# Kernel tuning notes

Hardware: AMD Instinct MI355X
Metric: run time of the kernel (lower is better)

Reference implementation:

```python
import jax, jax.numpy as jnp
import numpy as np

_POWERS = jnp.array([128, 64, 32, 16, 8, 4, 2, 1], dtype=jnp.int32)


def _unpack_ternary(pos_mask, neg_mask, in_dim):
    """Unpack uint8-style bitmasks [out, in//8] to ternary {-1,0,+1} [out, in]."""
    out_dim = pos_mask.shape[0]
    pos_bits = ((pos_mask[:, :, None] & _POWERS) != 0).astype(jnp.int8)  # [out, in/8, 8]
    neg_bits = ((neg_mask[:, :, None] & _POWERS) != 0).astype(jnp.int8)
    w_t = (pos_bits - neg_bits).reshape(out_dim, -1)[:, :in_dim]
    return w_t


def setup_inputs() -> dict:
    key = jax.random.key(0)
    k1, k2, k3, k4, k5 = jax.random.split(key, 5)
    TOKENS, IN, OUT = 4096, 4096, 4096
    x = jax.random.normal(k1, (TOKENS, IN), dtype=jnp.float32)
    pos_mask = jax.random.randint(k2, (OUT, IN // 8), 0, 256, dtype=jnp.int32)
    neg_mask = jax.random.randint(k3, (OUT, IN // 8), 0, 256, dtype=jnp.int32)
    scale = jax.random.uniform(k4, (), dtype=jnp.float32) * 0.05 + 0.01  # absmean scale
    bias = jax.random.normal(k5, (OUT,), dtype=jnp.float32)
    return {"x": x, "pos_mask": pos_mask, "neg_mask": neg_mask, "scale": scale,
            "bias": bias, "in_features": IN}


def reference(x, pos_mask, neg_mask, scale, bias, in_features):
    # y = scale * (x @ W_pos.T - x @ W_neg.T) + bias == scale * (x @ w_t.T) + bias,
    # since pos - neg == w_t exactly (entries in {-1,0,+1}).
    w_t = _unpack_ternary(pos_mask, neg_mask, in_features).astype(x.dtype)  # [out, in]
    y = scale * jnp.einsum('ti,oi->to', x, w_t) + bias
    return y
```

## Files before the change

### kernel.cpp

```cpp
#include <hip/hip_runtime.h>
#include <hip/hip_bf16.h>

typedef unsigned short ushort_t;
typedef unsigned int uint_t;

typedef __attribute__((ext_vector_type(8))) short bf16x8;
typedef __attribute__((ext_vector_type(4))) float f32x4;
typedef __attribute__((ext_vector_type(8))) unsigned short u16x8;

constexpr int Mdim = 4096;
constexpr int Ndim = 4096;
constexpr int Kdim = 4096;
constexpr int K2 = Kdim * 2;
constexpr int NIT = Kdim / 128;

__device__ __forceinline__ ushort_t f2bf(float f) {
  uint_t u = __float_as_uint(f);
  u += 0x7fffu + ((u >> 16) & 1u);
  return (ushort_t)(u >> 16);
}

__global__ void __launch_bounds__(256) cvt_x_kernel(const float* __restrict__ x,
                                                    ushort_t* __restrict__ xb) {
  const size_t t = (size_t)blockIdx.x * 256 + threadIdx.x;
  const float4* p = reinterpret_cast<const float4*>(x) + t * 2;
  float4 a = p[0], b = p[1];
  u16x8 o;
  o[0] = f2bf(a.x); o[1] = f2bf(a.y); o[2] = f2bf(a.z); o[3] = f2bf(a.w);
  o[4] = f2bf(b.x); o[5] = f2bf(b.y); o[6] = f2bf(b.z); o[7] = f2bf(b.w);
  *reinterpret_cast<u16x8*>(xb + t * 8) = o;
}

__global__ void __launch_bounds__(256) unpack_w_kernel(const int* __restrict__ pos,
                                                       const int* __restrict__ neg,
                                                       ushort_t* __restrict__ wb) {
  const size_t t = (size_t)blockIdx.x * 256 + threadIdx.x;
  const int4 p = reinterpret_cast<const int4*>(pos)[t];
  const int4 q = reinterpret_cast<const int4*>(neg)[t];
  const int pv[4] = {p.x, p.y, p.z, p.w};
  const int nv[4] = {q.x, q.y, q.z, q.w};
  ushort_t* dst = wb + t * 32;
#pragma unroll
  for (int e = 0; e < 4; ++e) {
    u16x8 v;
#pragma unroll
    for (int j = 0; j < 8; ++j) {
      const int pb = (pv[e] >> (7 - j)) & 1;
      const int nb = (nv[e] >> (7 - j)) & 1;
      const int d = pb - nb;
      v[j] = (d == 1) ? (ushort_t)0x3F80 : ((d == -1) ? (ushort_t)0xBF80 : (ushort_t)0);
    }
    *reinterpret_cast<u16x8*>(dst + e * 8) = v;
  }
}

#define GLD16(gp, lp)                                                     \
  __builtin_amdgcn_global_load_lds(                                       \
      (const __attribute__((address_space(1))) void*)(gp),                \
      (__attribute__((address_space(3))) void*)(lp), 16, 0, 0)

#define VMCNT(N) asm volatile("s_waitcnt vmcnt(" #N ")" ::: "memory")

#define BARRIER() do {                          \
  __builtin_amdgcn_sched_barrier(0);            \
  __builtin_amdgcn_s_barrier();                 \
  __builtin_amdgcn_sched_barrier(0);            \
} while (0)


#define STAGE_A(BUF, HALF, KT) do {                                                    \
  const char* g_ = Ab + gAoff + (size_t)(HALF) * (128 * (size_t)K2) + (size_t)(KT) * 128; \
  char* l_ = ldsw + (BUF) * 32768 + (HALF) * 16384;                                    \
  GLD16(g_, l_);                                                                       \
  GLD16(g_ + (size_t)64 * K2, l_ + 8192);                                              \
} while (0)

#define STAGE_B(BUF, HALF, KT) do {                                                    \
  const char* g_ = Bb + gBoff + (size_t)(HALF) * (128 * (size_t)K2) + (size_t)(KT) * 128; \
  char* l_ = ldsw + 65536 + (BUF) * 32768 + (HALF) * 16384;                            \
  GLD16(g_, l_);                                                                       \
  GLD16(g_ + (size_t)64 * K2, l_ + 8192);                                              \
} while (0)

#define LDA(BUF, M, KK) (*(const bf16x8*)(lds + (BUF) * 32768 + aRowBase + (M) * 2048 + acol[KK]))
#define LDB(BUF, N, KK) (*(const bf16x8*)(lds + 65536 + (BUF) * 32768 + bRowBase + (N) * 2048 + acol[KK]))

#define PHASE(BUF, Q, PREBAR2, ...) do {                                               \
  bf16x8 a0k0 = LDA(BUF, 2*(Q),   0), a0k1 = LDA(BUF, 2*(Q),   1);                     \
  bf16x8 a1k0 = LDA(BUF, 2*(Q)+1, 0), a1k1 = LDA(BUF, 2*(Q)+1, 1);                     \
  if ((Q) == 0) {                                                                      \
    _Pragma("unroll")                                                                  \
    for (int n_ = 0; n_ < 4; ++n_) { vb[n_][0] = LDB(BUF, n_, 0); vb[n_][1] = LDB(BUF, n_, 1); } \
  }                                                                                    \
  __VA_ARGS__;                                                                         \
  BARRIER();                                                                           \
  __builtin_amdgcn_s_setprio(1);                                                       \
  _Pragma("unroll")                                                                    \
  for (int n_ = 0; n_ < 4; ++n_) {                                                     \
    acc[2*(Q)][n_]   = __builtin_amdgcn_mfma_f32_16x16x32_bf16(a0k0, vb[n_][0], acc[2*(Q)][n_],   0, 0, 0); \
    acc[2*(Q)+1][n_] = __builtin_amdgcn_mfma_f32_16x16x32_bf16(a1k0, vb[n_][0], acc[2*(Q)+1][n_], 0, 0, 0); \
  }                                                                                    \
  _Pragma("unroll")                                                                    \
  for (int n_ = 0; n_ < 4; ++n_) {                                                     \
    acc[2*(Q)][n_]   = __builtin_amdgcn_mfma_f32_16x16x32_bf16(a0k1, vb[n_][1], acc[2*(Q)][n_],   0, 0, 0); \
    acc[2*(Q)+1][n_] = __builtin_amdgcn_mfma_f32_16x16x32_bf16(a1k1, vb[n_][1], acc[2*(Q)+1][n_], 0, 0, 0); \
  }                                                                                    \
  __builtin_amdgcn_s_setprio(0);                                                       \
  PREBAR2;                                                                             \
  BARRIER();                                                                           \
} while (0)

__global__ void __launch_bounds__(512, 2) gemm_kernel(const ushort_t* __restrict__ A,
                                                      const ushort_t* __restrict__ B,
                                                      float* __restrict__ C,
                                                      const float* __restrict__ scale_p,
                                                      const float* __restrict__ bias) {
  __shared__ char lds[131072];

  const int bid = blockIdx.x;
  const int swz = (bid & 7) * 32 + (bid >> 3);
  const int m0 = (swz >> 4) * 256;
  const int n0 = (swz & 15) * 256;

  const int tid = threadIdx.x;
  const int wid = tid >> 6;
  const int lane = tid & 63;
  const int wr = wid >> 2;
  const int wc = wid & 3;

  float sv = *scale_p;
  float bv[4];
#pragma unroll
  for (int n = 0; n < 4; ++n) bv[n] = bias[n0 + wc * 64 + n * 16 + (lane & 15)];
  asm volatile("" : "+v"(sv), "+v"(bv[0]), "+v"(bv[1]), "+v"(bv[2]), "+v"(bv[3]));

  const int srow = tid >> 3;
  const int scol = 16 * ((tid & 7) ^ (srow & 7));
  const char* Ab = (const char*)A;
  const char* Bb = (const char*)B;
  const size_t gAoff = (size_t)(m0 + srow) * K2 + scol;
  const size_t gBoff = (size_t)(n0 + srow) * K2 + scol;
  char* ldsw = lds + wid * 1024;

  const int acol[2] = { (0  + ((lane >> 4) << 4)) ^ ((lane & 7) << 4),
                        (64 + ((lane >> 4) << 4)) ^ ((lane & 7) << 4) };
  const int aRowBase = wr * 16384 + (lane & 15) * 128;
  const int bRowBase = (wc >> 1) * 16384 + ((wc & 1) * 64 + (lane & 15)) * 128;

  f32x4 acc[8][4] = {};
  bf16x8 vb[4][2];

  STAGE_B(0, 0, 0); STAGE_B(0, 1, 0);
  STAGE_A(0, 0, 0); STAGE_A(0, 1, 0);
  STAGE_B(1, 0, 1); STAGE_B(1, 1, 1);
  VMCNT(4);
  BARRIER();

#pragma unroll 1
  for (int i = 0; i < NIT - 1; ++i) {
    const int t0 = 2 * i, t1 = 2 * i + 1;
    PHASE(0, 0, ,      STAGE_A(1, 0, t1); STAGE_A(1, 1, t1));
    PHASE(0, 1, ,      STAGE_B(0, 0, t0 + 2));
    PHASE(0, 2, ,      STAGE_B(0, 1, t0 + 2));
    PHASE(0, 3, VMCNT(4), );
    PHASE(1, 0, ,      STAGE_A(0, 0, t0 + 2));
    PHASE(1, 1, ,      STAGE_A(0, 1, t0 + 2));
    PHASE(1, 2, ,      STAGE_B(1, 0, t1 + 2));
    PHASE(1, 3, VMCNT(4), STAGE_B(1, 1, t1 + 2));
  }
  {
    PHASE(0, 0, ,      STAGE_A(1, 0, 2 * NIT - 1); STAGE_A(1, 1, 2 * NIT - 1));
    PHASE(0, 1, , );
    PHASE(0, 2, , );
    PHASE(0, 3, VMCNT(0), );
    PHASE(1, 0, , );
    PHASE(1, 1, , );
    PHASE(1, 2, , );
    PHASE(1, 3, , );
  }

  const int row0 = m0 + wr * 128 + ((lane >> 4) << 2);
  const int col0 = n0 + wc * 64 + (lane & 15);
#pragma unroll
  for (int m = 0; m < 8; ++m)
#pragma unroll
    for (int n = 0; n < 4; ++n) {
      const int c = col0 + n * 16;
#pragma unroll
      for (int k = 0; k < 4; ++k)
        C[(size_t)(row0 + m * 16 + k) * Ndim + c] = sv * acc[m][n][k] + bv[n];
    }
}

extern "C" void kernel_launch(void* const* d_in, const int* in_sizes, int n_in,
                              void* d_out, int out_size, void* d_ws, size_t ws_size,
                              hipStream_t stream) {
  const float* x = (const float*)d_in[0];
  const int* pos = (const int*)d_in[1];
  const int* neg = (const int*)d_in[2];
  const float* scale = (const float*)d_in[3];
  const float* bias = (const float*)d_in[4];
  float* out = (float*)d_out;

  ushort_t* xb = (ushort_t*)d_ws;
  ushort_t* wb = xb + (size_t)Mdim * Kdim;

  cvt_x_kernel<<<(Mdim * Kdim) / (256 * 8), 256, 0, stream>>>(x, xb);
  unpack_w_kernel<<<(Ndim * (Kdim / 8)) / (256 * 4), 256, 0, stream>>>(pos, neg, wb);
  gemm_kernel<<<dim3((Mdim / 256) * (Ndim / 256)), 512, 0, stream>>>(xb, wb, out, scale, bias);
}
```

Before: 242.5 us.

## Double-buffer A fragments in registers to overlap LDS reads with MFMA

Restructures the GEMM main loop so the A fragments for the next phase are read from LDS into a second register bank while the MFMAs for the current phase run. This replaces the two-barrier-per-phase scheme with one barrier per phase and adjusts the vmcnt waits. It is meant to hide LDS read latency behind matrix compute and cut barrier overhead. The cost is extra VGPR pressure from the second fragment bank, plus some risk in the LDS buffer reuse ordering.

Result: no change. 239.9 us (-1.0%).

```diff
diff --git a/kernel.cpp b/kernel.cpp
--- a/kernel.cpp
+++ b/kernel.cpp
@@ -85,29 +85,29 @@
 #define LDA(BUF, M, KK) (*(const bf16x8*)(lds + (BUF) * 32768 + aRowBase + (M) * 2048 + acol[KK]))
 #define LDB(BUF, N, KK) (*(const bf16x8*)(lds + 65536 + (BUF) * 32768 + bRowBase + (N) * 2048 + acol[KK]))
 
-#define PHASE(BUF, Q, PREBAR2, ...) do {                                               \
-  bf16x8 a0k0 = LDA(BUF, 2*(Q),   0), a0k1 = LDA(BUF, 2*(Q),   1);                     \
-  bf16x8 a1k0 = LDA(BUF, 2*(Q)+1, 0), a1k1 = LDA(BUF, 2*(Q)+1, 1);                     \
-  if ((Q) == 0) {                                                                      \
-    _Pragma("unroll")                                                                  \
-    for (int n_ = 0; n_ < 4; ++n_) { vb[n_][0] = LDB(BUF, n_, 0); vb[n_][1] = LDB(BUF, n_, 1); } \
-  }                                                                                    \
-  __VA_ARGS__;                                                                         \
-  BARRIER();                                                                           \
+#define READS_A(BANK, RB, RQ) do {                                                     \
+  af##BANK[0] = LDA(RB, 2*(RQ),   0); af##BANK[1] = LDA(RB, 2*(RQ),   1);              \
+  af##BANK[2] = LDA(RB, 2*(RQ)+1, 0); af##BANK[3] = LDA(RB, 2*(RQ)+1, 1);              \
+} while (0)
+
+#define READS_B(CB) do {                                                               \
+  _Pragma("unroll")                                                                    \
+  for (int n_ = 0; n_ < 4; ++n_) { vb[n_][0] = LDB(CB, n_, 0); vb[n_][1] = LDB(CB, n_, 1); } \
+} while (0)
+
+#define MFMA16(BANK, Q) do {                                                           \
   __builtin_amdgcn_s_setprio(1);                                                       \
   _Pragma("unroll")                                                                    \
   for (int n_ = 0; n_ < 4; ++n_) {                                                     \
-    acc[2*(Q)][n_]   = __builtin_amdgcn_mfma_f32_16x16x32_bf16(a0k0, vb[n_][0], acc[2*(Q)][n_],   0, 0, 0); \
-    acc[2*(Q)+1][n_] = __builtin_amdgcn_mfma_f32_16x16x32_bf16(a1k0, vb[n_][0], acc[2*(Q)+1][n_], 0, 0, 0); \
+    acc[2*(Q)][n_]   = __builtin_amdgcn_mfma_f32_16x16x32_bf16(af##BANK[0], vb[n_][0], acc[2*(Q)][n_],   0, 0, 0); \
+    acc[2*(Q)+1][n_] = __builtin_amdgcn_mfma_f32_16x16x32_bf16(af##BANK[2], vb[n_][0], acc[2*(Q)+1][n_], 0, 0, 0); \
   }                                                                                    \
   _Pragma("unroll")                                                                    \
   for (int n_ = 0; n_ < 4; ++n_) {                                                     \
-    acc[2*(Q)][n_]   = __builtin_amdgcn_mfma_f32_16x16x32_bf16(a0k1, vb[n_][1], acc[2*(Q)][n_],   0, 0, 0); \
-    acc[2*(Q)+1][n_] = __builtin_amdgcn_mfma_f32_16x16x32_bf16(a1k1, vb[n_][1], acc[2*(Q)+1][n_], 0, 0, 0); \
+    acc[2*(Q)][n_]   = __builtin_amdgcn_mfma_f32_16x16x32_bf16(af##BANK[1], vb[n_][1], acc[2*(Q)][n_],   0, 0, 0); \
+    acc[2*(Q)+1][n_] = __builtin_amdgcn_mfma_f32_16x16x32_bf16(af##BANK[3], vb[n_][1], acc[2*(Q)+1][n_], 0, 0, 0); \
   }                                                                                    \
   __builtin_amdgcn_s_setprio(0);                                                       \
-  PREBAR2;                                                                             \
-  BARRIER();                                                                           \
 } while (0)
 
 __global__ void __launch_bounds__(512, 2) gemm_kernel(const ushort_t* __restrict__ A,
@@ -148,6 +148,7 @@
   const int bRowBase = (wc >> 1) * 16384 + ((wc & 1) * 64 + (lane & 15)) * 128;
 
   f32x4 acc[8][4] = {};
+  bf16x8 af0[4], af1[4];
   bf16x8 vb[4][2];
 
   STAGE_B(0, 0, 0); STAGE_B(0, 1, 0);
@@ -155,28 +156,40 @@
   STAGE_B(1, 0, 1); STAGE_B(1, 1, 1);
   VMCNT(4);
   BARRIER();
+  READS_A(0, 0, 0);
 
 #pragma unroll 1
   for (int i = 0; i < NIT - 1; ++i) {
-    const int t0 = 2 * i, t1 = 2 * i + 1;
-    PHASE(0, 0, ,      STAGE_A(1, 0, t1); STAGE_A(1, 1, t1));
-    PHASE(0, 1, ,      STAGE_B(0, 0, t0 + 2));
-    PHASE(0, 2, ,      STAGE_B(0, 1, t0 + 2));
-    PHASE(0, 3, VMCNT(4), );
-    PHASE(1, 0, ,      STAGE_A(0, 0, t0 + 2));
-    PHASE(1, 1, ,      STAGE_A(0, 1, t0 + 2));
-    PHASE(1, 2, ,      STAGE_B(1, 0, t1 + 2));
-    PHASE(1, 3, VMCNT(4), STAGE_B(1, 1, t1 + 2));
+    const int t1 = 2 * i + 1, tn = 2 * i + 2;
+    BARRIER(); STAGE_A(1, 0, t1); STAGE_A(1, 1, t1);
+               READS_B(0); READS_A(1, 0, 1); MFMA16(0, 0);
+    BARRIER(); STAGE_B(0, 0, tn);
+               READS_A(0, 0, 2); MFMA16(1, 1);
+    BARRIER(); STAGE_B(0, 1, tn);
+               READS_A(1, 0, 3); MFMA16(0, 2);
+    VMCNT(4);
+    BARRIER(); READS_A(0, 1, 0); MFMA16(1, 3);
+    BARRIER(); STAGE_A(0, 0, tn);
+               READS_B(1); READS_A(1, 1, 1); MFMA16(0, 0);
+    BARRIER(); STAGE_A(0, 1, tn);
+               READS_A(0, 1, 2); MFMA16(1, 1);
+    BARRIER(); STAGE_B(1, 0, t1 + 2);
+               READS_A(1, 1, 3); MFMA16(0, 2);
+    VMCNT(2);
+    BARRIER(); STAGE_B(1, 1, t1 + 2);
+               READS_A(0, 0, 0); MFMA16(1, 3);
   }
   {
-    PHASE(0, 0, ,      STAGE_A(1, 0, 2 * NIT - 1); STAGE_A(1, 1, 2 * NIT - 1));
-    PHASE(0, 1, , );
-    PHASE(0, 2, , );
-    PHASE(0, 3, VMCNT(0), );
-    PHASE(1, 0, , );
-    PHASE(1, 1, , );
-    PHASE(1, 2, , );
-    PHASE(1, 3, , );
+    BARRIER(); STAGE_A(1, 0, 2 * NIT - 1); STAGE_A(1, 1, 2 * NIT - 1);
+               READS_B(0); READS_A(1, 0, 1); MFMA16(0, 0);
+    BARRIER(); READS_A(0, 0, 2); MFMA16(1, 1);
+    BARRIER(); READS_A(1, 0, 3); MFMA16(0, 2);
+    VMCNT(0);
+    BARRIER(); READS_A(0, 1, 0); MFMA16(1, 3);
+    BARRIER(); READS_B(1); READS_A(1, 1, 1); MFMA16(0, 0);
+    BARRIER(); READS_A(0, 1, 2); MFMA16(1, 1);
+    BARRIER(); READS_A(1, 1, 3); MFMA16(0, 2);
+    BARRIER(); MFMA16(1, 3);
   }
 
   const int row0 = m0 + wr * 128 + ((lane >> 4) << 2);
```
